# Optimization experiments

Measured on AMD Instinct MI355X. Metric: run time of the kernel, lower is better.

Reference implementation:

```python
import jax, jax.numpy as jnp
import numpy as np

EMB_DIM = 1024
N_HEAD = 16
HEAD_DIM = EMB_DIM // N_HEAD


def setup_inputs() -> dict:
    key = jax.random.key(0)
    k1, k2, k3, k4, k5 = jax.random.split(key, 5)
    x = jax.random.normal(k1, (4, 2048, EMB_DIM), dtype=jnp.float32)
    s = 1.0 / np.sqrt(EMB_DIM)
    W_qkv = jax.random.uniform(k2, (3 * EMB_DIM, EMB_DIM), minval=-s, maxval=s, dtype=jnp.float32)
    b_qkv = jax.random.uniform(k3, (3 * EMB_DIM,), minval=-s, maxval=s, dtype=jnp.float32)
    W_proj = jax.random.uniform(k4, (EMB_DIM, EMB_DIM), minval=-s, maxval=s, dtype=jnp.float32)
    b_proj = jax.random.uniform(k5, (EMB_DIM,), minval=-s, maxval=s, dtype=jnp.float32)
    return {"x": x, "W_qkv": W_qkv, "b_qkv": b_qkv, "W_proj": W_proj, "b_proj": b_proj}


def reference(x, W_qkv, b_qkv, W_proj, b_proj):
    B, S, E = x.shape
    H, D = N_HEAD, HEAD_DIM
    qkv = x @ W_qkv.T + b_qkv  # [B,S,3E]
    q, k, v = jnp.split(qkv, 3, axis=-1)
    # [B,S,E] -> [B,H,S,D]
    q = q.reshape(B, S, H, D).transpose(0, 2, 1, 3)
    k = k.reshape(B, S, H, D).transpose(0, 2, 1, 3)
    v = v.reshape(B, S, H, D).transpose(0, 2, 1, 3)
    scale = 1.0 / jnp.sqrt(jnp.asarray(D, dtype=x.dtype))
    scores = jnp.einsum('bhqd,bhkd->bhqk', q, k) * scale
    causal = jnp.tril(jnp.ones((S, S), dtype=bool))
    scores = jnp.where(causal, scores, jnp.asarray(-jnp.inf, dtype=scores.dtype))
    attn = jax.nn.softmax(scores, axis=-1)
    y = jnp.einsum('bhqk,bhkd->bhqd', attn, v)  # [B,H,S,D]
    y = y.transpose(0, 2, 1, 3).reshape(B, S, E)
    return y @ W_proj.T + b_proj
```

## Files before the change

kernel.cpp:

```cpp
#include <hip/hip_runtime.h>
#include <hip/hip_bf16.h>

typedef __attribute__((ext_vector_type(4))) float f32x4;
typedef __attribute__((ext_vector_type(8))) __bf16 bf16x8;
typedef __attribute__((ext_vector_type(4))) unsigned int u32x4;

#define EMB 1024
#define NHEAD 16
#define HDIM 64
#define SEQ 2048
#define BATCH 4
#define NTOK 8192

__device__ __forceinline__ unsigned short f2bf(float f) {
    unsigned int u = __builtin_bit_cast(unsigned int, f);
    u = (u + 0x7fffu + ((u >> 16) & 1u)) >> 16;
    return (unsigned short)u;
}

__device__ __forceinline__ unsigned int pack_bf2(float lo, float hi) {
    unsigned int a = __builtin_bit_cast(unsigned int, lo);
    unsigned int b = __builtin_bit_cast(unsigned int, hi);
    return ((a + 0x8000u) >> 16) | ((b + 0x8000u) & 0xffff0000u);
}

__device__ __forceinline__ void async_copy16(const ushort* g, ushort* l) {
    __builtin_amdgcn_global_load_lds(
        (const __attribute__((address_space(1))) void*)g,
        (__attribute__((address_space(3))) void*)l,
        16, 0, 0);
}

__global__ void cvt_f32_bf16(const float4* __restrict__ in, ushort* __restrict__ out, int n4) {
    int i = blockIdx.x * 256 + threadIdx.x;
    if (i < n4) {
        float4 v = in[i];
        ushort4 o;
        o.x = f2bf(v.x); o.y = f2bf(v.y); o.z = f2bf(v.z); o.w = f2bf(v.w);
        ((ushort4*)out)[i] = o;
    }
}

#define GEMM_STAGE(Asrc, Bsrc, m0, n0, kt)                                        \
    {                                                                             \
        _Pragma("unroll")                                                         \
        for (int j = 0; j < 2; ++j) {                                             \
            int row = wave * 32 + j * 16 + (lane >> 2);                           \
            int kc  = (lane & 3) ^ ((row >> 1) & 3);                              \
            async_copy16(Asrc + (size_t)(m0 + row) * EMB + kt + kc * 8,           \
                         As + (wave * 32 + j * 16) * 32);                         \
            async_copy16(Bsrc + (size_t)(n0 + row) * EMB + kt + kc * 8,           \
                         Bs + (wave * 32 + j * 16) * 32);                         \
        }                                                                         \
    }

#define GEMM_BODY(Asrc, Bsrc, m0, n0)                                             \
    f32x4 acc[4][4] = {};                                                         \
    for (int kt = 0; kt < EMB; kt += 32) {                                        \
        GEMM_STAGE(Asrc, Bsrc, m0, n0, kt)                                        \
        __syncthreads();                                                          \
        bf16x8 a[4], b[4];                                                        \
        _Pragma("unroll")                                                         \
        for (int i = 0; i < 4; ++i) {                                             \
            int r = wm + i * 16 + col;                                            \
            a[i] = *(const bf16x8*)&As[r * 32 + (quad ^ ((r >> 1) & 3)) * 8];     \
            int c = wn + i * 16 + col;                                            \
            b[i] = *(const bf16x8*)&Bs[c * 32 + (quad ^ ((c >> 1) & 3)) * 8];     \
        }                                                                         \
        _Pragma("unroll")                                                         \
        for (int i = 0; i < 4; ++i)                                               \
            _Pragma("unroll")                                                     \
            for (int j = 0; j < 4; ++j)                                           \
                acc[i][j] = __builtin_amdgcn_mfma_f32_16x16x32_bf16(              \
                    a[i], b[j], acc[i][j], 0, 0, 0);                              \
        __syncthreads();                                                          \
    }

__global__ __launch_bounds__(256) void gemm_qk(
    const ushort* __restrict__ A,
    const ushort* __restrict__ W,
    const float*  __restrict__ bias,
    ushort* __restrict__ Qb, ushort* __restrict__ Kb)
{
    __shared__ ushort As[128 * 32];
    __shared__ ushort Bs[128 * 32];
    const int tid  = threadIdx.x;
    const int lane = tid & 63;
    const int wave = tid >> 6;
    const int col  = lane & 15;
    const int quad = lane >> 4;
    const int m0 = blockIdx.x * 128;
    const int n0 = blockIdx.y * 128;
    const int wm = (wave >> 1) * 64;
    const int wn = (wave & 1) * 64;

    GEMM_BODY(A, W, m0, n0)

    #pragma unroll
    for (int i = 0; i < 4; ++i)
        #pragma unroll
        for (int j = 0; j < 4; ++j)
            #pragma unroll
            for (int r = 0; r < 4; ++r) {
                int m = m0 + wm + i * 16 + quad * 4 + r;
                int n = n0 + wn + j * 16 + col;
                float v = acc[i][j][r] + bias[n];
                unsigned short bv = f2bf(v);
                int e = n & 1023;
                int h = e >> 6, d = e & 63;
                int b = m >> 11, s = m & 2047;
                size_t bh = (size_t)(b * NHEAD + h);
                if (n < 1024) Qb[(bh * SEQ + s) * HDIM + d] = bv;
                else          Kb[(bh * SEQ + s) * HDIM + d] = bv;
            }
}

__global__ __launch_bounds__(256) void gemm_vt(
    const ushort* __restrict__ Wv,
    const ushort* __restrict__ X,
    const float*  __restrict__ bias,
    ushort* __restrict__ Vtx)
{
    __shared__ ushort As[128 * 32];
    __shared__ ushort Bs[128 * 32];
    const int tid  = threadIdx.x;
    const int lane = tid & 63;
    const int wave = tid >> 6;
    const int col  = lane & 15;
    const int quad = lane >> 4;
    const int m0 = blockIdx.x * 128;
    const int n0 = blockIdx.y * 128;
    const int wm = (wave >> 1) * 64;
    const int wn = (wave & 1) * 64;

    GEMM_BODY(Wv, X, m0, n0)

    #pragma unroll
    for (int i = 0; i < 4; ++i)
        #pragma unroll
        for (int j = 0; j < 4; ++j)
            #pragma unroll
            for (int r = 0; r < 4; ++r) {
                int m = m0 + wm + i * 16 + quad * 4 + r;
                int n = n0 + wn + j * 16 + col;
                Vtx[(size_t)m * NTOK + n] = f2bf(acc[i][j][r] + bias[m]);
            }
}

__global__ __launch_bounds__(256) void gemm_proj(
    const ushort* __restrict__ A,
    const ushort* __restrict__ W,
    const float*  __restrict__ bias,
    float* __restrict__ out)
{
    __shared__ ushort As[128 * 32];
    __shared__ ushort Bs[128 * 32];
    const int tid  = threadIdx.x;
    const int lane = tid & 63;
    const int wave = tid >> 6;
    const int col  = lane & 15;
    const int quad = lane >> 4;
    const int m0 = blockIdx.x * 128;
    const int n0 = blockIdx.y * 128;
    const int wm = (wave >> 1) * 64;
    const int wn = (wave & 1) * 64;

    GEMM_BODY(A, W, m0, n0)

    #pragma unroll
    for (int i = 0; i < 4; ++i)
        #pragma unroll
        for (int j = 0; j < 4; ++j)
            #pragma unroll
            for (int r = 0; r < 4; ++r) {
                int m = m0 + wm + i * 16 + quad * 4 + r;
                int n = n0 + wn + j * 16 + col;
                out[(size_t)m * EMB + n] = acc[i][j][r] + bias[n];
            }
}

__device__ __forceinline__ void attn_qtile(
    int qb, int b, int h, int lane, int wave,
    const ushort* __restrict__ Qh, const ushort* __restrict__ Kh,
    const ushort* __restrict__ Vh, ushort* __restrict__ Yb,
    ushort* __restrict__ Ks0, ushort* __restrict__ Ks1, ushort* __restrict__ Vs)
{
    const int col  = lane & 15;
    const int quad = lane >> 4;
    const int q0  = qb * 64 + wave * 16;
    const int row = q0 + col;
    const float SC = 0.125f * 1.44269504f;
    const int addr0 = (col + 32 * (quad & 1)) * 4;
    const int addr1 = addr0 + 64;
    const bool hi = quad >= 2;

    bf16x8 qf0 = *(const bf16x8*)(Qh + (q0 + col) * HDIM + quad * 8);
    bf16x8 qf1 = *(const bf16x8*)(Qh + (q0 + col) * HDIM + 32 + quad * 8);

    f32x4 o[4] = {};
    float lrun = 0.f;

    const int nk = (qb >> 1) + 1;
    for (int kt = 0; kt < nk; ++kt) {
        const int k0 = kt * 128;
        const bool last = (kt == nk - 1);

        {
            int srow = wave * 16 + (lane >> 2);
            #pragma unroll
            for (int rr = 0; rr < 2; ++rr) {
                int r = rr * 64 + srow;
                int kc = (lane & 3) ^ ((r >> 1) & 3);
                const ushort* src = Kh + (size_t)(k0 + r) * HDIM + kc * 8;
                async_copy16(src,      Ks0 + (rr * 64 + wave * 16) * 32);
                async_copy16(src + 32, Ks1 + (rr * 64 + wave * 16) * 32);
            }
            int kc = (lane & 3) ^ ((srow >> 1) & 3);
            const ushort* vsrc = Vh + (size_t)srow * NTOK + k0 + kc * 8;
            #pragma unroll
            for (int kq = 0; kq < 4; ++kq)
                async_copy16(vsrc + kq * 32, Vs + kq * 2048 + (wave * 16) * 32);
        }
        __syncthreads();

        f32x4 st[8];
        #pragma unroll
        for (int j = 0; j < 8; ++j) {
            int r = j * 16 + col;
            int q_ = (quad ^ ((r >> 1) & 3)) * 8;
            bf16x8 kf0 = *(const bf16x8*)&Ks0[r * 32 + q_];
            bf16x8 kf1 = *(const bf16x8*)&Ks1[r * 32 + q_];
            f32x4 z = {0.f, 0.f, 0.f, 0.f};
            st[j] = __builtin_amdgcn_mfma_f32_16x16x32_bf16(kf0, qf0, z, 0, 0, 0);
            st[j] = __builtin_amdgcn_mfma_f32_16x16x32_bf16(kf1, qf1, st[j], 0, 0, 0);
        }

        #pragma unroll
        for (int j = 0; j < 8; ++j)
            #pragma unroll
            for (int r = 0; r < 4; ++r) {
                float pv = exp2f(st[j][r] * SC);
                if (last) {
                    int c = k0 + j * 16 + quad * 4 + r;
                    pv = (c <= row) ? pv : 0.f;
                }
                st[j][r] = pv;
                lrun += pv;
            }

        bf16x8 pf[4];
        #pragma unroll
        for (int g = 0; g < 2; ++g) {
            unsigned int pk[4][2];
            #pragma unroll
            for (int j = 0; j < 4; ++j) {
                pk[j][0] = pack_bf2(st[g * 4 + j][0], st[g * 4 + j][1]);
                pk[j][1] = pack_bf2(st[g * 4 + j][2], st[g * 4 + j][3]);
            }
            u32x4 ua, ub;
            int b00 = __builtin_amdgcn_ds_bpermute(addr0, (int)pk[0][0]);
            int b01 = __builtin_amdgcn_ds_bpermute(addr0, (int)pk[0][1]);
            int b02 = __builtin_amdgcn_ds_bpermute(addr1, (int)pk[0][0]);
            int b03 = __builtin_amdgcn_ds_bpermute(addr1, (int)pk[0][1]);
            int b10 = __builtin_amdgcn_ds_bpermute(addr0, (int)pk[1][0]);
            int b11 = __builtin_amdgcn_ds_bpermute(addr0, (int)pk[1][1]);
            int b12 = __builtin_amdgcn_ds_bpermute(addr1, (int)pk[1][0]);
            int b13 = __builtin_amdgcn_ds_bpermute(addr1, (int)pk[1][1]);
            ua[0] = hi ? b10 : b00; ua[1] = hi ? b11 : b01;
            ua[2] = hi ? b12 : b02; ua[3] = hi ? b13 : b03;
            int c00 = __builtin_amdgcn_ds_bpermute(addr0, (int)pk[2][0]);
            int c01 = __builtin_amdgcn_ds_bpermute(addr0, (int)pk[2][1]);
            int c02 = __builtin_amdgcn_ds_bpermute(addr1, (int)pk[2][0]);
            int c03 = __builtin_amdgcn_ds_bpermute(addr1, (int)pk[2][1]);
            int c10 = __builtin_amdgcn_ds_bpermute(addr0, (int)pk[3][0]);
            int c11 = __builtin_amdgcn_ds_bpermute(addr0, (int)pk[3][1]);
            int c12 = __builtin_amdgcn_ds_bpermute(addr1, (int)pk[3][0]);
            int c13 = __builtin_amdgcn_ds_bpermute(addr1, (int)pk[3][1]);
            ub[0] = hi ? c10 : c00; ub[1] = hi ? c11 : c01;
            ub[2] = hi ? c12 : c02; ub[3] = hi ? c13 : c03;
            pf[g * 2]     = __builtin_bit_cast(bf16x8, ua);
            pf[g * 2 + 1] = __builtin_bit_cast(bf16x8, ub);
        }

        #pragma unroll
        for (int dt = 0; dt < 4; ++dt) {
            int r = dt * 16 + col;
            int q_ = (quad ^ ((r >> 1) & 3)) * 8;
            #pragma unroll
            for (int kq = 0; kq < 4; ++kq) {
                bf16x8 vf = *(const bf16x8*)&Vs[kq * 2048 + r * 32 + q_];
                o[dt] = __builtin_amdgcn_mfma_f32_16x16x32_bf16(vf, pf[kq], o[dt], 0, 0, 0);
            }
        }
        __syncthreads();
    }

    lrun += __shfl_xor(lrun, 16, 64);
    lrun += __shfl_xor(lrun, 32, 64);
    float inv = 1.f / lrun;
    size_t rbase = ((size_t)(b * SEQ + row)) * EMB + h * HDIM + quad * 4;
    #pragma unroll
    for (int dt = 0; dt < 4; ++dt) {
        ushort4 s4;
        s4.x = f2bf(o[dt][0] * inv);
        s4.y = f2bf(o[dt][1] * inv);
        s4.z = f2bf(o[dt][2] * inv);
        s4.w = f2bf(o[dt][3] * inv);
        *(ushort4*)(Yb + rbase + dt * 16) = s4;
    }
}

__global__ __launch_bounds__(256, 4) void attn(
    const ushort* __restrict__ Qb, const ushort* __restrict__ Kb,
    const ushort* __restrict__ Vtx, ushort* __restrict__ Yb)
{
    __shared__ ushort Ks0[128 * 32];
    __shared__ ushort Ks1[128 * 32];
    __shared__ ushort Vs[4 * 64 * 32];
    const int lane = threadIdx.x & 63;
    const int wave = threadIdx.x >> 6;
    const int bh   = blockIdx.x & 63;
    const int pr   = blockIdx.x >> 6;

    const int b = bh >> 4, h = bh & 15;
    const ushort* Qh = Qb + (size_t)bh * SEQ * HDIM;
    const ushort* Kh = Kb + (size_t)bh * SEQ * HDIM;
    const ushort* Vh = Vtx + (size_t)(h * HDIM) * NTOK + b * SEQ;

    attn_qtile(31 - pr, b, h, lane, wave, Qh, Kh, Vh, Yb, Ks0, Ks1, Vs);
    __syncthreads();
    attn_qtile(pr,      b, h, lane, wave, Qh, Kh, Vh, Yb, Ks0, Ks1, Vs);
}

extern "C" void kernel_launch(void* const* d_in, const int* in_sizes, int n_in,
                              void* d_out, int out_size, void* d_ws, size_t ws_size,
                              hipStream_t stream) {
    const float* x      = (const float*)d_in[0];
    const float* W_qkv  = (const float*)d_in[1];
    const float* b_qkv  = (const float*)d_in[2];
    const float* W_proj = (const float*)d_in[3];
    const float* b_proj = (const float*)d_in[4];
    float* out = (float*)d_out;

    ushort* ws     = (ushort*)d_ws;
    ushort* Xb     = ws;
    ushort* Yb     = ws;
    ushort* Wqkvb  = ws + 8388608;
    ushort* Wprojb = ws + 11534336;
    ushort* Qb     = ws + 12582912;
    ushort* Kb     = ws + 20971520;
    ushort* Vtx    = ws + 29360128;

    cvt_f32_bf16<<<8192, 256, 0, stream>>>((const float4*)x,      Xb,     2097152);
    cvt_f32_bf16<<<3072, 256, 0, stream>>>((const float4*)W_qkv,  Wqkvb,  786432);
    cvt_f32_bf16<<<1024, 256, 0, stream>>>((const float4*)W_proj, Wprojb, 262144);

    gemm_qk<<<dim3(64, 16), 256, 0, stream>>>(Xb, Wqkvb, b_qkv, Qb, Kb);
    gemm_vt<<<dim3(8, 64), 256, 0, stream>>>(Wqkvb + (size_t)2048 * EMB, Xb,
                                             b_qkv + 2048, Vtx);
    attn<<<1024, 256, 0, stream>>>(Qb, Kb, Vtx, Yb);
    gemm_proj<<<dim3(64, 8), 256, 0, stream>>>(Yb, Wprojb, b_proj, out);
}
```

Before: 282.6 us.

## Split attention work across waves by key columns and fold softmax scale into Q

Each wave now owns a 32-key slice of every 128-key tile and handles all 64 query rows, so each K and V fragment is read from shared memory once and reused across four query sub-tiles. Partial outputs and row sums are combined across waves through a shared-memory reduction at the end. The softmax scale and log2e factor are folded into Q during the QKV GEMM epilogue, which removes a multiply per score. The change costs a four-way cross-wave reduction with extra barriers, more accumulator registers (launch bound lowered from 4 to 2 blocks), and rounding Q to bf16 after scaling.

```diff
diff --git a/kernel.cpp b/kernel.cpp
--- a/kernel.cpp
+++ b/kernel.cpp
@@ -104,7 +104,8 @@
             for (int r = 0; r < 4; ++r) {
                 int m = m0 + wm + i * 16 + quad * 4 + r;
                 int n = n0 + wn + j * 16 + col;
-                float v = acc[i][j][r] + bias[n];
+                float scl = (n < 1024) ? 0.18033688f : 1.0f;
+                float v = (acc[i][j][r] + bias[n]) * scl;
                 unsigned short bv = f2bf(v);
                 int e = n & 1023;
                 int h = e >> 6, d = e & 63;
@@ -183,22 +184,26 @@
     int qb, int b, int h, int lane, int wave,
     const ushort* __restrict__ Qh, const ushort* __restrict__ Kh,
     const ushort* __restrict__ Vh, ushort* __restrict__ Yb,
-    ushort* __restrict__ Ks0, ushort* __restrict__ Ks1, ushort* __restrict__ Vs)
+    ushort* __restrict__ Ks0, ushort* __restrict__ Ks1,
+    ushort* __restrict__ Vs, float* __restrict__ scratch, float* __restrict__ lrb)
 {
     const int col  = lane & 15;
     const int quad = lane >> 4;
-    const int q0  = qb * 64 + wave * 16;
-    const int row = q0 + col;
-    const float SC = 0.125f * 1.44269504f;
+    const int q0   = qb * 64;
     const int addr0 = (col + 32 * (quad & 1)) * 4;
     const int addr1 = addr0 + 64;
     const bool hi = quad >= 2;
 
-    bf16x8 qf0 = *(const bf16x8*)(Qh + (q0 + col) * HDIM + quad * 8);
-    bf16x8 qf1 = *(const bf16x8*)(Qh + (q0 + col) * HDIM + 32 + quad * 8);
-
-    f32x4 o[4] = {};
-    float lrun = 0.f;
+    bf16x8 qf[4][2];
+    #pragma unroll
+    for (int qs = 0; qs < 4; ++qs) {
+        const ushort* qp = Qh + (q0 + qs * 16 + col) * HDIM + quad * 8;
+        qf[qs][0] = *(const bf16x8*)(qp);
+        qf[qs][1] = *(const bf16x8*)(qp + 32);
+    }
+
+    f32x4 o[4][4] = {};
+    float lr[4] = {};
 
     const int nk = (qb >> 1) + 1;
     for (int kt = 0; kt < nk; ++kt) {
@@ -223,100 +228,126 @@
         }
         __syncthreads();
 
-        f32x4 st[8];
-        #pragma unroll
-        for (int j = 0; j < 8; ++j) {
-            int r = j * 16 + col;
+        bf16x8 kf0[2], kf1[2];
+        #pragma unroll
+        for (int j2 = 0; j2 < 2; ++j2) {
+            int r = (wave * 2 + j2) * 16 + col;
             int q_ = (quad ^ ((r >> 1) & 3)) * 8;
-            bf16x8 kf0 = *(const bf16x8*)&Ks0[r * 32 + q_];
-            bf16x8 kf1 = *(const bf16x8*)&Ks1[r * 32 + q_];
-            f32x4 z = {0.f, 0.f, 0.f, 0.f};
-            st[j] = __builtin_amdgcn_mfma_f32_16x16x32_bf16(kf0, qf0, z, 0, 0, 0);
-            st[j] = __builtin_amdgcn_mfma_f32_16x16x32_bf16(kf1, qf1, st[j], 0, 0, 0);
-        }
-
-        #pragma unroll
-        for (int j = 0; j < 8; ++j)
-            #pragma unroll
-            for (int r = 0; r < 4; ++r) {
-                float pv = exp2f(st[j][r] * SC);
-                if (last) {
-                    int c = k0 + j * 16 + quad * 4 + r;
-                    pv = (c <= row) ? pv : 0.f;
-                }
-                st[j][r] = pv;
-                lrun += pv;
-            }
-
-        bf16x8 pf[4];
-        #pragma unroll
-        for (int g = 0; g < 2; ++g) {
-            unsigned int pk[4][2];
-            #pragma unroll
-            for (int j = 0; j < 4; ++j) {
-                pk[j][0] = pack_bf2(st[g * 4 + j][0], st[g * 4 + j][1]);
-                pk[j][1] = pack_bf2(st[g * 4 + j][2], st[g * 4 + j][3]);
-            }
-            u32x4 ua, ub;
-            int b00 = __builtin_amdgcn_ds_bpermute(addr0, (int)pk[0][0]);
-            int b01 = __builtin_amdgcn_ds_bpermute(addr0, (int)pk[0][1]);
-            int b02 = __builtin_amdgcn_ds_bpermute(addr1, (int)pk[0][0]);
-            int b03 = __builtin_amdgcn_ds_bpermute(addr1, (int)pk[0][1]);
-            int b10 = __builtin_amdgcn_ds_bpermute(addr0, (int)pk[1][0]);
-            int b11 = __builtin_amdgcn_ds_bpermute(addr0, (int)pk[1][1]);
-            int b12 = __builtin_amdgcn_ds_bpermute(addr1, (int)pk[1][0]);
-            int b13 = __builtin_amdgcn_ds_bpermute(addr1, (int)pk[1][1]);
-            ua[0] = hi ? b10 : b00; ua[1] = hi ? b11 : b01;
-            ua[2] = hi ? b12 : b02; ua[3] = hi ? b13 : b03;
-            int c00 = __builtin_amdgcn_ds_bpermute(addr0, (int)pk[2][0]);
-            int c01 = __builtin_amdgcn_ds_bpermute(addr0, (int)pk[2][1]);
-            int c02 = __builtin_amdgcn_ds_bpermute(addr1, (int)pk[2][0]);
-            int c03 = __builtin_amdgcn_ds_bpermute(addr1, (int)pk[2][1]);
-            int c10 = __builtin_amdgcn_ds_bpermute(addr0, (int)pk[3][0]);
-            int c11 = __builtin_amdgcn_ds_bpermute(addr0, (int)pk[3][1]);
-            int c12 = __builtin_amdgcn_ds_bpermute(addr1, (int)pk[3][0]);
-            int c13 = __builtin_amdgcn_ds_bpermute(addr1, (int)pk[3][1]);
-            ub[0] = hi ? c10 : c00; ub[1] = hi ? c11 : c01;
-            ub[2] = hi ? c12 : c02; ub[3] = hi ? c13 : c03;
-            pf[g * 2]     = __builtin_bit_cast(bf16x8, ua);
-            pf[g * 2 + 1] = __builtin_bit_cast(bf16x8, ub);
-        }
-
+            kf0[j2] = *(const bf16x8*)&Ks0[r * 32 + q_];
+            kf1[j2] = *(const bf16x8*)&Ks1[r * 32 + q_];
+        }
+        bf16x8 vf[4];
         #pragma unroll
         for (int dt = 0; dt < 4; ++dt) {
             int r = dt * 16 + col;
             int q_ = (quad ^ ((r >> 1) & 3)) * 8;
-            #pragma unroll
-            for (int kq = 0; kq < 4; ++kq) {
-                bf16x8 vf = *(const bf16x8*)&Vs[kq * 2048 + r * 32 + q_];
-                o[dt] = __builtin_amdgcn_mfma_f32_16x16x32_bf16(vf, pf[kq], o[dt], 0, 0, 0);
-            }
+            vf[dt] = *(const bf16x8*)&Vs[wave * 2048 + r * 32 + q_];
+        }
+
+        #pragma unroll
+        for (int qs = 0; qs < 4; ++qs) {
+            f32x4 st[2];
+            #pragma unroll
+            for (int j2 = 0; j2 < 2; ++j2) {
+                f32x4 z = {0.f, 0.f, 0.f, 0.f};
+                st[j2] = __builtin_amdgcn_mfma_f32_16x16x32_bf16(kf0[j2], qf[qs][0], z, 0, 0, 0);
+                st[j2] = __builtin_amdgcn_mfma_f32_16x16x32_bf16(kf1[j2], qf[qs][1], st[j2], 0, 0, 0);
+            }
+            #pragma unroll
+            for (int j2 = 0; j2 < 2; ++j2)
+                #pragma unroll
+                for (int r = 0; r < 4; ++r) {
+                    float pv = exp2f(st[j2][r]);
+                    if (last) {
+                        int c = k0 + (wave * 2 + j2) * 16 + quad * 4 + r;
+                        int rowq = q0 + qs * 16 + col;
+                        pv = (c <= rowq) ? pv : 0.f;
+                    }
+                    st[j2][r] = pv;
+                    lr[qs] += pv;
+                }
+            unsigned int pk0[2], pk1[2];
+            #pragma unroll
+            for (int j2 = 0; j2 < 2; ++j2) {
+                pk0[j2] = pack_bf2(st[j2][0], st[j2][1]);
+                pk1[j2] = pack_bf2(st[j2][2], st[j2][3]);
+            }
+            u32x4 ua;
+            int b00 = __builtin_amdgcn_ds_bpermute(addr0, (int)pk0[0]);
+            int b01 = __builtin_amdgcn_ds_bpermute(addr0, (int)pk1[0]);
+            int b02 = __builtin_amdgcn_ds_bpermute(addr1, (int)pk0[0]);
+            int b03 = __builtin_amdgcn_ds_bpermute(addr1, (int)pk1[0]);
+            int b10 = __builtin_amdgcn_ds_bpermute(addr0, (int)pk0[1]);
+            int b11 = __builtin_amdgcn_ds_bpermute(addr0, (int)pk1[1]);
+            int b12 = __builtin_amdgcn_ds_bpermute(addr1, (int)pk0[1]);
+            int b13 = __builtin_amdgcn_ds_bpermute(addr1, (int)pk1[1]);
+            ua[0] = hi ? b10 : b00; ua[1] = hi ? b11 : b01;
+            ua[2] = hi ? b12 : b02; ua[3] = hi ? b13 : b03;
+            bf16x8 pf = __builtin_bit_cast(bf16x8, ua);
+
+            #pragma unroll
+            for (int dt = 0; dt < 4; ++dt)
+                o[dt][qs] = __builtin_amdgcn_mfma_f32_16x16x32_bf16(vf[dt], pf, o[dt][qs], 0, 0, 0);
         }
         __syncthreads();
     }
 
-    lrun += __shfl_xor(lrun, 16, 64);
-    lrun += __shfl_xor(lrun, 32, 64);
-    float inv = 1.f / lrun;
-    size_t rbase = ((size_t)(b * SEQ + row)) * EMB + h * HDIM + quad * 4;
-    #pragma unroll
-    for (int dt = 0; dt < 4; ++dt) {
-        ushort4 s4;
-        s4.x = f2bf(o[dt][0] * inv);
-        s4.y = f2bf(o[dt][1] * inv);
-        s4.z = f2bf(o[dt][2] * inv);
-        s4.w = f2bf(o[dt][3] * inv);
-        *(ushort4*)(Yb + rbase + dt * 16) = s4;
-    }
-}
-
-__global__ __launch_bounds__(256, 4) void attn(
+    #pragma unroll
+    for (int qs = 0; qs < 4; ++qs) {
+        lr[qs] += __shfl_xor(lr[qs], 16, 64);
+        lr[qs] += __shfl_xor(lr[qs], 32, 64);
+    }
+    if (quad == 0) {
+        #pragma unroll
+        for (int qs = 0; qs < 4; ++qs)
+            lrb[wave * 64 + qs * 16 + col] = lr[qs];
+    }
+    float linv = 0.f;
+    #pragma unroll
+    for (int half = 0; half < 2; ++half) {
+        #pragma unroll
+        for (int dd = 0; dd < 2; ++dd) {
+            int dt = half * 2 + dd;
+            #pragma unroll
+            for (int qs = 0; qs < 4; ++qs)
+                *(f32x4*)&scratch[(((wave * 2 + dd) * 64) + qs * 16 + col) * 16 + quad * 4] = o[dt][qs];
+        }
+        __syncthreads();
+        if (half == 0) {
+            float lt = lrb[0 * 64 + wave * 16 + col] + lrb[1 * 64 + wave * 16 + col]
+                     + lrb[2 * 64 + wave * 16 + col] + lrb[3 * 64 + wave * 16 + col];
+            linv = 1.f / lt;
+        }
+        #pragma unroll
+        for (int dd = 0; dd < 2; ++dd) {
+            int dt = half * 2 + dd;
+            f32x4 sum = {0.f, 0.f, 0.f, 0.f};
+            #pragma unroll
+            for (int sw = 0; sw < 4; ++sw)
+                sum += *(const f32x4*)&scratch[(((sw * 2 + dd) * 64) + wave * 16 + col) * 16 + quad * 4];
+            int srow = q0 + wave * 16 + col;
+            ushort4 s4;
+            s4.x = f2bf(sum[0] * linv);
+            s4.y = f2bf(sum[1] * linv);
+            s4.z = f2bf(sum[2] * linv);
+            s4.w = f2bf(sum[3] * linv);
+            *(ushort4*)(Yb + ((size_t)(b * SEQ + srow)) * EMB + h * HDIM + dt * 16 + quad * 4) = s4;
+        }
+        __syncthreads();
+    }
+}
+
+__global__ __launch_bounds__(256, 2) void attn(
     const ushort* __restrict__ Qb, const ushort* __restrict__ Kb,
     const ushort* __restrict__ Vtx, ushort* __restrict__ Yb)
 {
-    __shared__ ushort Ks0[128 * 32];
-    __shared__ ushort Ks1[128 * 32];
-    __shared__ ushort Vs[4 * 64 * 32];
+    __shared__ ushort lds_raw[16384 + 512];
+    ushort* Ks0 = lds_raw;
+    ushort* Ks1 = lds_raw + 4096;
+    ushort* Vs  = lds_raw + 8192;
+    float* scratch = (float*)lds_raw;
+    float* lrb = (float*)(lds_raw + 16384);
+
     const int lane = threadIdx.x & 63;
     const int wave = threadIdx.x >> 6;
     const int bh   = blockIdx.x & 63;
@@ -327,9 +358,9 @@
     const ushort* Kh = Kb + (size_t)bh * SEQ * HDIM;
     const ushort* Vh = Vtx + (size_t)(h * HDIM) * NTOK + b * SEQ;
 
-    attn_qtile(31 - pr, b, h, lane, wave, Qh, Kh, Vh, Yb, Ks0, Ks1, Vs);
+    attn_qtile(31 - pr, b, h, lane, wave, Qh, Kh, Vh, Yb, Ks0, Ks1, Vs, scratch, lrb);
     __syncthreads();
-    attn_qtile(pr,      b, h, lane, wave, Qh, Kh, Vh, Yb, Ks0, Ks1, Vs);
+    attn_qtile(pr,      b, h, lane, wave, Qh, Kh, Vh, Yb, Ks0, Ks1, Vs, scratch, lrb);
 }
 
 extern "C" void kernel_launch(void* const* d_in, const int* in_sizes, int n_in,
```

Measured after the change: 294.2 us. +4.1%, slower.
